# Optimization experiments

Measured on AMD Instinct MI355X. Metric: run time of the kernel, lower is better.

## Reference

```python
import jax, jax.numpy as jnp
import numpy as np

N, D, C, K, M = 32768, 512, 64, 16, 128
DEPTH = 4            # log2(K): decision-tree depth per codebook
NODES = K - 1        # 15 internal tree nodes per codebook


def _build_selection_matrix():
    # Node i of the binary tree lives at level log2(i+1) and thresholds the
    # level-l selected dimension of its codebook.
    S = np.zeros((C * NODES, C * DEPTH), dtype=np.float32)
    base = np.zeros((NODES, DEPTH), dtype=np.float32)
    for i in range(NODES):
        base[i, int(np.log2(i + 1))] = 1.0
    for c in range(C):
        S[c * NODES:(c + 1) * NODES, c * DEPTH:(c + 1) * DEPTH] = base
    return S


def _build_bit_matrix():
    # Leaf k scores +1/-1 on each of its DEPTH ancestor nodes; the true leaf
    # attains the maximal score DEPTH.
    base = np.zeros((K, NODES), dtype=np.float32)
    for k in range(K):
        for l in range(DEPTH):
            node = (1 << l) - 1 + (k >> (DEPTH - l))   # ancestor at level l
            bit = (k >> (DEPTH - 1 - l)) & 1            # right(1)/left(0)
            base[k, node] = 1.0 if bit else -1.0
    B = np.zeros((C * K, C * NODES), dtype=np.float32)
    for c in range(C):
        B[c * K:(c + 1) * K, c * NODES:(c + 1) * NODES] = base
    return B


def setup_inputs() -> dict:
    key = jax.random.key(0)
    k1, k2, k3, k4 = jax.random.split(key, 4)
    I = jax.random.normal(k1, (N, D), jnp.float32)
    T = jax.random.normal(k2, (C * NODES,), jnp.float32) * 0.1   # thresholds
    L = jax.random.normal(k3, (M, C, K), jnp.float32)            # LUT
    dims = jnp.sort(jax.random.randint(k4, (C * DEPTH,), 0, D))  # selected cols
    S = jnp.asarray(_build_selection_matrix())
    B = jnp.asarray(_build_bit_matrix())
    temp = jnp.ones((1,), jnp.float32)
    return {"I": I, "T": T, "L": L, "S": S, "B": B, "dims": dims, "temp": temp}


def reference(I, T, L, S, B, dims, temp):
    t = temp[0]
    x_sel = I[:, dims]                                  # (N, C*DEPTH) gather
    h = x_sel @ S.T - T                                 # (N, C*NODES)
    tanh_h = jnp.tanh(h / t)
    # straight-through sign: forward sign(h), backward d(tanh(h/t))
    sign_ste = jnp.sign(h) - jax.lax.stop_gradient(tanh_h) + tanh_h
    b = sign_ste @ B.T                                  # (N, C*K) leaf scores
    soft = jax.nn.softmax(b.reshape(-1, C, K) / t, axis=2)
    hard = jax.nn.one_hot(jnp.argmax(soft, axis=2), K, dtype=soft.dtype)
    # straight-through one-hot encoding E: forward hard, backward soft
    E = hard - jax.lax.stop_gradient(soft) + soft       # (N, C, K)
    return jnp.einsum("nck,mck->nm", E, L)              # LUT gather-sum readout
```

## Files before the change

kernel.cpp:

```cpp
#include <hip/hip_runtime.h>

#define N_TOTAL 32768
#define D_DIM   512
#define C_DIM   64
#define K_DIM   16
#define M_DIM   128
#define NODES_  15
#define ROWS    16

typedef unsigned short u16;
typedef unsigned int   u32;

__device__ __forceinline__ u32 f2bf_bits(float f) {
    u32 u = __float_as_uint(f);
    return (u + 0x7FFFu + ((u >> 16) & 1u)) >> 16;
}
__device__ __forceinline__ float bf_lo(u32 u) { return __uint_as_float(u << 16); }
__device__ __forceinline__ float bf_hi(u32 u) { return __uint_as_float(u & 0xFFFF0000u); }

__global__ __launch_bounds__(256) void build_lut_kernel(
    const float* __restrict__ L, u16* __restrict__ LUT)
{
    int idx = blockIdx.x * 256 + threadIdx.x;
    int q  = idx & 15;
    int kk = (idx >> 4) & 255;
    int p  = idx >> 12;
    int c0 = (2 * p) * 16 + (kk & 15);
    int c1 = (2 * p + 1) * 16 + (kk >> 4);
    u32 w[4];
    #pragma unroll
    for (int h = 0; h < 4; ++h) {
        int m0 = q * 8 + 2 * h;
        float a0 = L[m0 * 1024 + c0]       + L[m0 * 1024 + c1];
        float a1 = L[(m0 + 1) * 1024 + c0] + L[(m0 + 1) * 1024 + c1];
        w[h] = f2bf_bits(a0) | (f2bf_bits(a1) << 16);
    }
    *(uint4*)(LUT + (size_t)((p << 8) | kk) * M_DIM + q * 8) =
        make_uint4(w[0], w[1], w[2], w[3]);
}

__global__ __launch_bounds__(256) void fused_kernel(
    const float* __restrict__ I,
    const float* __restrict__ T,
    const int* __restrict__ dims,
    const u16* __restrict__ LUT,
    float* __restrict__ out)
{
    __shared__ float sT[C_DIM * NODES_];

    const int tid  = threadIdx.x;
    const int lane = tid & 63;
    const int wv   = tid >> 6;
    const int rowBase = blockIdx.x * ROWS + wv * 4;

    const int4 dml = ((const int4*)dims)[lane];

    float vv[4][4];
    #pragma unroll
    for (int rr = 0; rr < 4; ++rr) {
        const float* v = I + (size_t)(rowBase + rr) * D_DIM;
        vv[rr][0] = v[dml.x];
        vv[rr][1] = v[dml.y];
        vv[rr][2] = v[dml.z];
        vv[rr][3] = v[dml.w];
    }

    for (int j = tid; j < C_DIM * NODES_; j += 256) sT[j] = T[j];
    __syncthreads();

    const float* tc = sT + lane * NODES_;
    u32 cp = 0;
    #pragma unroll
    for (int rr = 0; rr < 4; ++rr) {
        int node = 0, k = 0;
        #pragma unroll
        for (int l = 0; l < 4; ++l) {
            float h = vv[rr][l] - tc[node];
            int bit = (h > 0.0f) ? 1 : 0;
            k = (k << 1) | bit;
            node = (node << 1) + 1 + bit;
        }
        cp |= (u32)k << (4 * rr);
    }

    const int r   = lane >> 4;
    const int q   = lane & 15;
    const int rsh = r * 4;

    float4 acc0 = make_float4(0.f, 0.f, 0.f, 0.f);
    float4 acc1 = make_float4(0.f, 0.f, 0.f, 0.f);

    #pragma unroll
    for (int p = 0; p < 32; ++p) {
        u32 ca = (u32)__builtin_amdgcn_readlane((int)cp, 2 * p);
        u32 cb = (u32)__builtin_amdgcn_readlane((int)cp, 2 * p + 1);
        u32 kk = ((ca >> rsh) & 15u) | (((cb >> rsh) & 15u) << 4);
        const uint4 v = *(const uint4*)(LUT + (((p << 8) | kk) << 7) + (q << 3));
        acc0.x += bf_lo(v.x); acc0.y += bf_hi(v.x);
        acc0.z += bf_lo(v.y); acc0.w += bf_hi(v.y);
        acc1.x += bf_lo(v.z); acc1.y += bf_hi(v.z);
        acc1.z += bf_lo(v.w); acc1.w += bf_hi(v.w);
    }

    float4* o = (float4*)(out + (size_t)(rowBase + r) * M_DIM + (q << 3));
    o[0] = acc0;
    o[1] = acc1;
}

extern "C" void kernel_launch(void* const* d_in, const int* in_sizes, int n_in,
                              void* d_out, int out_size, void* d_ws, size_t ws_size,
                              hipStream_t stream) {
    const float* I    = (const float*)d_in[0];
    const float* T    = (const float*)d_in[1];
    const float* L    = (const float*)d_in[2];
    const int*   dims = (const int*)d_in[5];

    u16* LUT = (u16*)d_ws;

    hipLaunchKernelGGL(build_lut_kernel, dim3(512), dim3(256), 0, stream, L, LUT);
    hipLaunchKernelGGL(fused_kernel, dim3(N_TOTAL / ROWS), dim3(256), 0, stream,
                       I, T, dims, LUT, (float*)d_out);
}
```

Baseline: 126.4 us.

## Split into code-computation and one-hot MFMA GEMM kernels for LUT readout

```diff
diff --git a/kernel.cpp b/kernel.cpp
--- a/kernel.cpp
+++ b/kernel.cpp
@@ -6,63 +6,63 @@
 #define K_DIM   16
 #define M_DIM   128
 #define NODES_  15
-#define ROWS    16
 
 typedef unsigned short u16;
 typedef unsigned int   u32;
+typedef unsigned long long u64;
+typedef unsigned char  u8;
+typedef float  f32x4  __attribute__((ext_vector_type(4)));
+typedef short  short8v __attribute__((ext_vector_type(8)));
 
 __device__ __forceinline__ u32 f2bf_bits(float f) {
     u32 u = __float_as_uint(f);
     return (u + 0x7FFFu + ((u >> 16) & 1u)) >> 16;
 }
-__device__ __forceinline__ float bf_lo(u32 u) { return __uint_as_float(u << 16); }
-__device__ __forceinline__ float bf_hi(u32 u) { return __uint_as_float(u & 0xFFFF0000u); }
 
-__global__ __launch_bounds__(256) void build_lut_kernel(
-    const float* __restrict__ L, u16* __restrict__ LUT)
-{
-    int idx = blockIdx.x * 256 + threadIdx.x;
-    int q  = idx & 15;
-    int kk = (idx >> 4) & 255;
-    int p  = idx >> 12;
-    int c0 = (2 * p) * 16 + (kk & 15);
-    int c1 = (2 * p + 1) * 16 + (kk >> 4);
-    u32 w[4];
-    #pragma unroll
-    for (int h = 0; h < 4; ++h) {
-        int m0 = q * 8 + 2 * h;
-        float a0 = L[m0 * 1024 + c0]       + L[m0 * 1024 + c1];
-        float a1 = L[(m0 + 1) * 1024 + c0] + L[(m0 + 1) * 1024 + c1];
-        w[h] = f2bf_bits(a0) | (f2bf_bits(a1) << 16);
-    }
-    *(uint4*)(LUT + (size_t)((p << 8) | kk) * M_DIM + q * 8) =
-        make_uint4(w[0], w[1], w[2], w[3]);
+__device__ __forceinline__ void gload_lds4(const float* g, float* l) {
+    __builtin_amdgcn_global_load_lds(
+        (const __attribute__((address_space(1))) void*)g,
+        (__attribute__((address_space(3))) void*)l, 4, 0, 0);
 }
 
-__global__ __launch_bounds__(256) void fused_kernel(
+__global__ __launch_bounds__(256) void build_lb(
+    const float* __restrict__ L, u16* __restrict__ Lb)
+{
+    int i0 = (blockIdx.x * 256 + threadIdx.x) * 8;
+    float4 a = *(const float4*)(L + i0);
+    float4 b = *(const float4*)(L + i0 + 4);
+    u32 w0 = f2bf_bits(a.x) | (f2bf_bits(a.y) << 16);
+    u32 w1 = f2bf_bits(a.z) | (f2bf_bits(a.w) << 16);
+    u32 w2 = f2bf_bits(b.x) | (f2bf_bits(b.y) << 16);
+    u32 w3 = f2bf_bits(b.z) | (f2bf_bits(b.w) << 16);
+    *(uint4*)(Lb + i0) = make_uint4(w0, w1, w2, w3);
+}
+
+__global__ __launch_bounds__(256) void codes_kernel(
     const float* __restrict__ I,
     const float* __restrict__ T,
     const int* __restrict__ dims,
-    const u16* __restrict__ LUT,
-    float* __restrict__ out)
+    u8* __restrict__ cws)
 {
+    __shared__ float sIg[16 * 256];
     __shared__ float sT[C_DIM * NODES_];
 
     const int tid  = threadIdx.x;
     const int lane = tid & 63;
     const int wv   = tid >> 6;
-    const int rowBase = blockIdx.x * ROWS + wv * 4;
+    const int rowBase = blockIdx.x * 16 + wv * 4;
 
-    const int4 dml = ((const int4*)dims)[lane];
+    int dlv[4];
+    #pragma unroll
+    for (int i = 0; i < 4; ++i) dlv[i] = dims[i * 64 + lane];
 
-    float vv[4][4];
     #pragma unroll
     for (int rr = 0; rr < 4; ++rr) {
-        const float* v = I + (size_t)(rowBase + rr) * D_DIM;
-        vv[rr][0] = v[dml.x];
-        vv[rr][1] = v[dml.y];
-        vv[rr][2] = v[dml.z];
-        vv[rr][3] = v[dml.w];
+        const float* src = I + (size_t)(rowBase + rr) * D_DIM;
+        float* dst = sIg + (wv * 4 + rr) * 256;
+        #pragma unroll
+        for (int i = 0; i < 4; ++i)
+            gload_lds4(src + dlv[i], dst + i * 64);
     }
 
     for (int j = tid; j < C_DIM * NODES_; j += 256) sT[j] = T[j];
@@ -72,39 +72,88 @@
     u32 cp = 0;
     #pragma unroll
     for (int rr = 0; rr < 4; ++rr) {
+        const float4 x = *(const float4*)(sIg + (wv * 4 + rr) * 256 + lane * 4);
         int node = 0, k = 0;
-        #pragma unroll
-        for (int l = 0; l < 4; ++l) {
-            float h = vv[rr][l] - tc[node];
-            int bit = (h > 0.0f) ? 1 : 0;
-            k = (k << 1) | bit;
-            node = (node << 1) + 1 + bit;
-        }
+        int b0 = (x.x - tc[0] > 0.0f) ? 1 : 0;
+        k = b0; node = 1 + b0;
+        int b1 = (x.y - tc[node] > 0.0f) ? 1 : 0;
+        k = (k << 1) | b1; node = (node << 1) + 1 + b1;
+        int b2 = (x.z - tc[node] > 0.0f) ? 1 : 0;
+        k = (k << 1) | b2; node = (node << 1) + 1 + b2;
+        int b3 = (x.w - tc[node] > 0.0f) ? 1 : 0;
+        k = (k << 1) | b3;
         cp |= (u32)k << (4 * rr);
     }
 
-    const int r   = lane >> 4;
-    const int q   = lane & 15;
-    const int rsh = r * 4;
+    u32 cw =  (cp & 0xFu)
+           | ((cp >> 4)  & 0xFu) << 8
+           | ((cp >> 8)  & 0xFu) << 16
+           | ((cp >> 12) & 0xFu) << 24;
+    *(u32*)(cws + (size_t)lane * N_TOTAL + rowBase) = cw;
+}
 
-    float4 acc0 = make_float4(0.f, 0.f, 0.f, 0.f);
-    float4 acc1 = make_float4(0.f, 0.f, 0.f, 0.f);
+__global__ __launch_bounds__(256) void gemm_kernel(
+    const u16* __restrict__ Lb,
+    const u8* __restrict__ cws,
+    float* __restrict__ out)
+{
+    __shared__ u8 sC[C_DIM * 64];
+
+    const int tid  = threadIdx.x;
+    const int lane = tid & 63;
+    const int wv   = tid >> 6;
+    const int rowBase = blockIdx.x * 64;
+
+    {
+        int cls = tid >> 2, off = (tid & 3) * 16;
+        *(uint4*)(sC + cls * 64 + off) =
+            *(const uint4*)(cws + (size_t)cls * N_TOTAL + rowBase + off);
+    }
+    __syncthreads();
+
+    const int l15     = lane & 15;
+    const int clsLane = (lane >> 5) & 1;
+    const int kb      = ((lane >> 4) & 1) * 8;
+
+    f32x4 acc[4][2] = {};
+
+    const u16* lb0 = Lb + (size_t)((wv * 2 + 0) * 16 + l15) * 1024 + ((lane >> 4) * 8);
+    const u16* lb1 = Lb + (size_t)((wv * 2 + 1) * 16 + l15) * 1024 + ((lane >> 4) * 8);
+
+    #pragma unroll 4
+    for (int ch = 0; ch < 32; ++ch) {
+        union { uint4 u; short8v v; } b0, b1;
+        b0.u = *(const uint4*)(lb0 + ch * 32);
+        b1.u = *(const uint4*)(lb1 + ch * 32);
+        const int cls = ch * 2 + clsLane;
+        #pragma unroll
+        for (int rt = 0; rt < 4; ++rt) {
+            u32 cd = sC[cls * 64 + rt * 16 + l15];
+            u32 tt = cd - (u32)kb;
+            u64 sv = 0x3F80ull << ((tt & 3) * 16);
+            union { u64 d[2]; short8v v; } a;
+            a.d[0] = (tt < 4) ? sv : 0ull;
+            a.d[1] = (tt >= 4 && tt < 8) ? sv : 0ull;
+            acc[rt][0] = __builtin_amdgcn_mfma_f32_16x16x32_bf16(
+                             a.v, b0.v, acc[rt][0], 0, 0, 0);
+            acc[rt][1] = __builtin_amdgcn_mfma_f32_16x16x32_bf16(
+                             a.v, b1.v, acc[rt][1], 0, 0, 0);
+        }
+    }
 
     #pragma unroll
-    for (int p = 0; p < 32; ++p) {
-        u32 ca = (u32)__builtin_amdgcn_readlane((int)cp, 2 * p);
-        u32 cb = (u32)__builtin_amdgcn_readlane((int)cp, 2 * p + 1);
-        u32 kk = ((ca >> rsh) & 15u) | (((cb >> rsh) & 15u) << 4);
-        const uint4 v = *(const uint4*)(LUT + (((p << 8) | kk) << 7) + (q << 3));
-        acc0.x += bf_lo(v.x); acc0.y += bf_hi(v.x);
-        acc0.z += bf_lo(v.y); acc0.w += bf_hi(v.y);
-        acc1.x += bf_lo(v.z); acc1.y += bf_hi(v.z);
-        acc1.z += bf_lo(v.w); acc1.w += bf_hi(v.w);
+    for (int rt = 0; rt < 4; ++rt) {
+        #pragma unroll
+        for (int cj = 0; cj < 2; ++cj) {
+            int col = (wv * 2 + cj) * 16 + l15;
+            int r0  = rowBase + rt * 16 + ((lane >> 4) << 2);
+            float* o = out + (size_t)r0 * M_DIM + col;
+            o[0 * M_DIM] = acc[rt][cj][0];
+            o[1 * M_DIM] = acc[rt][cj][1];
+            o[2 * M_DIM] = acc[rt][cj][2];
+            o[3 * M_DIM] = acc[rt][cj][3];
+        }
     }
-
-    float4* o = (float4*)(out + (size_t)(rowBase + r) * M_DIM + (q << 3));
-    o[0] = acc0;
-    o[1] = acc1;
 }
 
 extern "C" void kernel_launch(void* const* d_in, const int* in_sizes, int n_in,
@@ -115,9 +164,12 @@
     const float* L    = (const float*)d_in[2];
     const int*   dims = (const int*)d_in[5];
 
-    u16* LUT = (u16*)d_ws;
+    u16* Lb = (u16*)d_ws;
+    u8*  cw = (u8*)d_ws + (1 << 18);
 
-    hipLaunchKernelGGL(build_lut_kernel, dim3(512), dim3(256), 0, stream, L, LUT);
-    hipLaunchKernelGGL(fused_kernel, dim3(N_TOTAL / ROWS), dim3(256), 0, stream,
-                       I, T, dims, LUT, (float*)d_out);
+    hipLaunchKernelGGL(build_lb,   dim3(64),   dim3(256), 0, stream, L, Lb);
+    hipLaunchKernelGGL(codes_kernel, dim3(N_TOTAL / 16), dim3(256), 0, stream,
+                       I, T, dims, cw);
+    hipLaunchKernelGGL(gemm_kernel, dim3(N_TOTAL / 64), dim3(256), 0, stream,
+                       Lb, cw, (float*)d_out);
 }
```

New measurement: 132.1 us. +4.5%, slower.
